# Performance work log

Hardware: AMD Instinct MI355X
Metric: run time of the kernel (lower is better)

## Reference

```python
import jax, jax.numpy as jnp
import numpy as np
import math

B, L, IN, HID, NLAYERS, AA = 16, 512, 512, 512, 6, 21
KAPPA_ADD = 5.0


def _sru_layer(x, W, v, b):
    # x: [L, B, din]; W: [din, 2*HID*k]; v, b: [2(gate f/r), 2(dir), HID]
    Lx, Bx, din = x.shape
    d = HID
    k = W.shape[1] // (2 * d)  # 4 if projecting residual, 3 if residual = input
    U = (x @ W).reshape(Lx, Bx, 2, d, k)
    res = U[..., 3] if k == 4 else x.reshape(Lx, Bx, 2, d)
    # time-flip direction 1 so a single scan handles both directions
    flip = lambda a: jnp.concatenate([a[:, :, :1], a[::-1, :, 1:]], axis=2)
    u0, u1, u2, resf = flip(U[..., 0]), flip(U[..., 1]), flip(U[..., 2]), flip(res)
    vf, vr = v[0], v[1]
    bf, br = b[0], b[1]

    def step(c, t):
        u0t, u1t, u2t, rt = t
        f = jax.nn.sigmoid(u1t + vf * c + bf)
        c1 = f * c + (1.0 - f) * u0t
        r = jax.nn.sigmoid(u2t + vr * c1 + br)
        h = r * c1 + (1.0 - r) * rt
        return c1, h

    c0 = jnp.zeros((Bx, 2, d), x.dtype)
    _, H = jax.lax.scan(step, c0, (u0, u1, u2, resf))
    return flip(H).reshape(Lx, Bx, 2 * d)


def setup_inputs():
    key = jax.random.key(0)
    inp = {}
    inp['input'] = jax.random.normal(jax.random.fold_in(key, 0), (B, L, IN), jnp.float32)
    inp['hidden'] = jnp.zeros((NLAYERS, B, 2 * HID), jnp.float32)
    for l in range(NLAYERS):
        din = IN if l == 0 else 2 * HID
        k = 4 if din != 2 * HID else 3
        inp[f'sru_w{l}'] = jax.random.normal(jax.random.fold_in(key, 10 + l), (din, 2 * HID * k), jnp.float32) * (1.0 / math.sqrt(din))
        inp[f'sru_v{l}'] = jax.random.normal(jax.random.fold_in(key, 20 + l), (2, 2, HID), jnp.float32) * 0.1
        inp[f'sru_b{l}'] = jnp.zeros((2, 2, HID), jnp.float32)

    def lin(seed, din, dout):
        w = jax.random.normal(jax.random.fold_in(key, seed), (din, dout), jnp.float32) * (1.0 / math.sqrt(din))
        return w, jnp.zeros((dout,), jnp.float32)

    inp['fc1_logits_w'], inp['fc1_logits_b'] = lin(30, 2 * HID, HID)
    inp['fc2_logits_w'], inp['fc2_logits_b'] = lin(31, HID, AA)
    inp['fc1_angles_w'], inp['fc1_angles_b'] = lin(32, 2 * HID, HID)
    inp['fc2_means_w'], inp['fc2_means_b'] = lin(33, HID, 2)
    inp['fc2_kappas_w'], inp['fc2_kappas_b'] = lin(34, HID, 2)
    return inp


def reference(input, hidden, sru_w0, sru_v0, sru_b0, sru_w1, sru_v1, sru_b1, sru_w2, sru_v2, sru_b2, sru_w3, sru_v3, sru_b3, sru_w4, sru_v4, sru_b4, sru_w5, sru_v5, sru_b5, fc1_logits_w, fc1_logits_b, fc2_logits_w, fc2_logits_b, fc1_angles_w, fc1_angles_b, fc2_means_w, fc2_means_b, fc2_kappas_w, fc2_kappas_b):
    x = input.transpose(1, 0, 2)  # [L, B, IN]
    ws = [sru_w0, sru_w1, sru_w2, sru_w3, sru_w4, sru_w5]
    vs = [sru_v0, sru_v1, sru_v2, sru_v3, sru_v4, sru_v5]
    bs = [sru_b0, sru_b1, sru_b2, sru_b3, sru_b4, sru_b5]
    for W, v, b in zip(ws, vs, bs):
        x = _sru_layer(x, W, v, b)
    sru_out = x.transpose(1, 0, 2)  # [B, L, 2*HID]
    h_log = sru_out @ fc1_logits_w + fc1_logits_b
    output_logits = jax.nn.log_softmax(h_log @ fc2_logits_w + fc2_logits_b, axis=-1)
    h_ang = sru_out @ fc1_angles_w + fc1_angles_b
    output_means = jnp.tanh(h_ang @ fc2_means_w + fc2_means_b) * math.pi
    output_kappas = KAPPA_ADD + jax.nn.softplus(h_ang @ fc2_kappas_w + fc2_kappas_b)
    return (output_logits, output_means, output_kappas)
```

## Files before the change

kernel.cpp:

```cpp
#include <hip/hip_runtime.h>

typedef __attribute__((ext_vector_type(8))) short short8;
typedef __attribute__((ext_vector_type(4))) float f32x4;

__device__ __forceinline__ ushort f2bf(float x) {
  unsigned u = __builtin_bit_cast(unsigned, x);
  u = (u + 0x7fffu + ((u >> 16) & 1u)) >> 16;
  return (ushort)u;
}
__device__ __forceinline__ float bf2f(ushort x) {
  return __builtin_bit_cast(float, ((unsigned)x) << 16);
}

#define AS1CP(p) ((const __attribute__((address_space(1))) unsigned int*)(p))
#define AS3CP(p) ((__attribute__((address_space(3))) unsigned int*)(p))
#define GLDS(g, l, SZ) __builtin_amdgcn_global_load_lds(AS1CP(g), AS3CP(l), SZ, 0, 0)

__global__ __launch_bounds__(256) void k_cvt(const float* __restrict__ in,
                                             ushort* __restrict__ out, int n4) {
  int i = blockIdx.x * 256 + threadIdx.x;
  if (i >= n4) return;
  float4 v = reinterpret_cast<const float4*>(in)[i];
  ushort4 o;
  o.x = f2bf(v.x); o.y = f2bf(v.y); o.z = f2bf(v.z); o.w = f2bf(v.w);
  reinterpret_cast<ushort4*>(out)[i] = o;
}

__global__ __launch_bounds__(256) void k_transpose(const float* __restrict__ W,
                                                   ushort* __restrict__ Wt,
                                                   int N, int K) {
  __shared__ float tile[32][33];
  int bx = blockIdx.x * 32;
  int by = blockIdx.y * 32;
  int tx = threadIdx.x, ty = threadIdx.y;
#pragma unroll
  for (int i = 0; i < 32; i += 8)
    tile[ty + i][tx] = W[(size_t)(by + ty + i) * N + bx + tx];
  __syncthreads();
#pragma unroll
  for (int i = 0; i < 32; i += 8)
    Wt[(size_t)(bx + ty + i) * K + by + tx] = f2bf(tile[tx][ty + i]);
}

template <int KKp>
__global__ __launch_bounds__(256) void k_transpose_sru(const float* __restrict__ W,
                                                       ushort* __restrict__ Wt,
                                                       int N, int K) {
  __shared__ float tile[32][33];
  int bx = blockIdx.x * 32;
  int by = blockIdx.y * 32;
  int tx = threadIdx.x, ty = threadIdx.y;
#pragma unroll
  for (int i = 0; i < 32; i += 8)
    tile[ty + i][tx] = W[(size_t)(by + ty + i) * N + bx + tx];
  __syncthreads();
#pragma unroll
  for (int i = 0; i < 32; i += 8) {
    int c = bx + ty + i;
    int ch = c / KKp, j = c - ch * KKp;
    int nc = (j < 2) ? (ch * 2 + j) : ((j == 2) ? (2048 + ch) : (3072 + ch));
    Wt[(size_t)nc * K + by + tx] = f2bf(tile[tx][ty + i]);
  }
}

template <int BF16OUT>
__global__ __launch_bounds__(256) void k_gemm(const ushort* __restrict__ A,
                                              const ushort* __restrict__ Bt,
                                              void* __restrict__ Cv,
                                              int K, int N) {
  __shared__ __align__(16) ushort lsA[2][4096];
  __shared__ __align__(16) ushort lsB[2][4096];
  const int tid = threadIdx.x;
  const int bm = blockIdx.x, bn = blockIdx.y;
  const int w = tid >> 6, l = tid & 63;
  const int wm = (w >> 1) * 64, wn = (w & 1) * 64;
  const int lr = l & 15, lg = l >> 4;
  f32x4 acc[4][4] = {};
  const int srow = tid >> 2;
  const int scol = (((tid & 3) ^ ((srow >> 1) & 3))) * 8;
  const ushort* Ag = A + (size_t)(bm * 128 + srow) * K + scol;
  const ushort* Bg = Bt + (size_t)(bn * 128 + srow) * K + scol;
  const int nt = K >> 5;
  const int rxor = (lr >> 1) & 3;

#define GEMM_ISSUE(BUF, KT)                                       \
  {                                                               \
    GLDS(Ag + (KT), &lsA[BUF][w * 512], 16);                      \
    GLDS(Ag + (size_t)64 * K + (KT), &lsA[BUF][2048 + w * 512], 16); \
    GLDS(Bg + (KT), &lsB[BUF][w * 512], 16);                      \
    GLDS(Bg + (size_t)64 * K + (KT), &lsB[BUF][2048 + w * 512], 16); \
  }

  GEMM_ISSUE(0, 0);
  for (int t = 0; t < nt; ++t) {
    const int cur = t & 1;
    if (t + 1 < nt) {
      GEMM_ISSUE(cur ^ 1, (t + 1) * 32);
      asm volatile("s_waitcnt vmcnt(4)" ::: "memory");
    } else {
      asm volatile("s_waitcnt vmcnt(0)" ::: "memory");
    }
    asm volatile("s_barrier" ::: "memory");
    short8 af[4], bfr[4];
#pragma unroll
    for (int i = 0; i < 4; ++i)
      af[i] = *(const short8*)&lsA[cur][(wm + i * 16 + lr) * 32 + ((lg ^ rxor) * 8)];
#pragma unroll
    for (int j = 0; j < 4; ++j)
      bfr[j] = *(const short8*)&lsB[cur][(wn + j * 16 + lr) * 32 + ((lg ^ rxor) * 8)];
#pragma unroll
    for (int i = 0; i < 4; ++i)
#pragma unroll
      for (int j = 0; j < 4; ++j)
        acc[i][j] = __builtin_amdgcn_mfma_f32_16x16x32_bf16(af[i], bfr[j], acc[i][j], 0, 0, 0);
    asm volatile("s_barrier" ::: "memory");
  }
#undef GEMM_ISSUE
  const size_t cbase = (size_t)(bm * 128 + wm + lg * 4) * N + bn * 128 + wn + lr;
  if (BF16OUT) {
    ushort* Cb = (ushort*)Cv + cbase;
#pragma unroll
    for (int i = 0; i < 4; ++i)
#pragma unroll
      for (int j = 0; j < 4; ++j)
#pragma unroll
        for (int r = 0; r < 4; ++r)
          Cb[(size_t)(i * 16 + r) * N + j * 16] = f2bf(acc[i][j][r]);
  } else {
    float* Cb = (float*)Cv + cbase;
#pragma unroll
    for (int i = 0; i < 4; ++i)
#pragma unroll
      for (int j = 0; j < 4; ++j)
#pragma unroll
        for (int r = 0; r < 4; ++r)
          Cb[(size_t)(i * 16 + r) * N + j * 16] = acc[i][j][r];
  }
}

__global__ __launch_bounds__(64, 1) void sru_rec6(const ushort* __restrict__ U, int NU,
                                                  const ushort* __restrict__ R, int RS,
                                                  const float* __restrict__ v,
                                                  const float* __restrict__ bb,
                                                  ushort* __restrict__ H) {
  const int lane = threadIdx.x;
  if (lane >= 16) return;
  const int blk = blockIdx.x;
  const int b = blk >> 6, rem = blk & 63, dir = rem >> 5;
  const int ch = dir * 512 + ((rem & 31) << 4) + lane;
  const float vf = v[ch], vr = v[1024 + ch];
  const float bfv = bb[ch], brv = bb[1024 + ch];
  const float vfn = -vf, vrn = -vr;
  const float kf0 = -bfv, kr0 = -brv;
  const int tstep = dir ? -1 : 1;
  const int t0 = dir ? 511 : 0;
  const ushort* U01 = U + (size_t)b * 512 * NU + ch * 2;
  const ushort* U2  = U + (size_t)b * 512 * NU + 2048 + ch;
  const ushort* Rb  = R + (size_t)b * 512 * RS + ch;
  ushort* Hb = H + (size_t)b * 512 * 1024 + ch;

  unsigned q01[4][8];
  ushort q2[4][8], qr[4][8];

#define SR_ISSUE(J, TI)                                                        \
  {                                                                            \
    const int base_ = (TI) * 8;                                                \
    _Pragma("unroll")                                                          \
    for (int t = 0; t < 8; ++t) {                                              \
      int tt = t0 + tstep * (base_ + t);                                       \
      q01[J][t] = *(const unsigned*)(U01 + (size_t)tt * NU);                   \
      q2[J][t] = U2[(size_t)tt * NU];                                          \
      qr[J][t] = Rb[(size_t)tt * RS];                                          \
    }                                                                          \
  }

#define SR_COMP(J, TI)                                                         \
  {                                                                            \
    _Pragma("unroll")                                                          \
    for (int s = 0; s < 8; ++s) {                                              \
      float u0 = bf2f((ushort)(q01[J][s] & 0xffffu));                          \
      float u1 = bf2f((ushort)(q01[J][s] >> 16));                              \
      float u2 = bf2f(q2[J][s]);                                               \
      float uR = bf2f(qr[J][s]);                                               \
      float ef = __expf(__builtin_fmaf(vfn, c, kf0 - u1));                     \
      float f = __builtin_amdgcn_rcpf(1.f + ef);                               \
      c = __builtin_fmaf(f, c - u0, u0);                                       \
      float er = __expf(__builtin_fmaf(vrn, c, kr0 - u2));                     \
      float r = __builtin_amdgcn_rcpf(1.f + er);                               \
      float hh = __builtin_fmaf(r, c - uR, uR);                                \
      Hb[(size_t)(t0 + tstep * ((TI) * 8 + s)) * 1024] = f2bf(hh);             \
    }                                                                          \
  }

#define SR_W32 asm volatile("s_waitcnt vmcnt(32)" ::: "memory");

  SR_ISSUE(0, 0)
  SR_ISSUE(1, 1)
  float c = 0.f;
  asm volatile("s_waitcnt vmcnt(24)" ::: "memory");
  SR_ISSUE(2, 2) SR_COMP(0, 0)
  SR_W32 SR_ISSUE(3, 3) SR_COMP(1, 1)
  SR_W32 SR_ISSUE(0, 4) SR_COMP(2, 2)
  SR_W32 SR_ISSUE(1, 5) SR_COMP(3, 3)
#pragma unroll 1
  for (int ii = 1; ii <= 14; ++ii) {
#define TILE_J(J)                                                              \
    {                                                                          \
      const int i = ii * 4 + (J);                                              \
      SR_W32                                                                   \
      SR_ISSUE((((J) + 2) & 3), i + 2)                                         \
      SR_COMP(J, i)                                                            \
    }
    TILE_J(0) TILE_J(1) TILE_J(2) TILE_J(3)
#undef TILE_J
  }
  SR_W32 SR_ISSUE(2, 62) SR_COMP(0, 60)
  SR_W32 SR_ISSUE(3, 63) SR_COMP(1, 61)
  SR_W32 SR_COMP(2, 62)
  asm volatile("s_waitcnt vmcnt(8)" ::: "memory");
  SR_COMP(3, 63)
#undef SR_ISSUE
#undef SR_COMP
#undef SR_W32
}

__global__ __launch_bounds__(256) void k_buildW2(const float* __restrict__ w2l,
                                                 const float* __restrict__ w2m,
                                                 const float* __restrict__ w2k,
                                                 ushort* __restrict__ Wt2) {
  int i = blockIdx.x * 256 + threadIdx.x;
  if (i >= 128 * 1024) return;
  int n = i >> 10, k = i & 1023;
  float vv = 0.f;
  if (n < 21 && k < 512) vv = w2l[k * 21 + n];
  else if (n >= 21 && n < 23 && k >= 512) vv = w2m[(k - 512) * 2 + (n - 21)];
  else if (n >= 23 && n < 25 && k >= 512) vv = w2k[(k - 512) * 2 + (n - 23)];
  Wt2[i] = f2bf(vv);
}

__global__ __launch_bounds__(64) void k_bias25(const float* __restrict__ b1l,
                                               const float* __restrict__ b1a,
                                               const float* __restrict__ w2l,
                                               const float* __restrict__ b2l,
                                               const float* __restrict__ w2m,
                                               const float* __restrict__ b2m,
                                               const float* __restrict__ w2k,
                                               const float* __restrict__ b2k,
                                               float* __restrict__ b2adj) {
  int o = threadIdx.x;
  if (o >= 25) return;
  float s;
  if (o < 21) {
    s = b2l[o];
    for (int k = 0; k < 512; ++k) s += b1l[k] * w2l[k * 21 + o];
  } else if (o < 23) {
    s = b2m[o - 21];
    for (int k = 0; k < 512; ++k) s += b1a[k] * w2m[k * 2 + (o - 21)];
  } else {
    s = b2k[o - 23];
    for (int k = 0; k < 512; ++k) s += b1a[k] * w2k[k * 2 + (o - 23)];
  }
  b2adj[o] = s;
}

__global__ __launch_bounds__(64) void k_act(const float* __restrict__ T,
                                            const float* __restrict__ b2adj,
                                            float* __restrict__ out) {
  const int row = blockIdx.x;
  const int lane = threadIdx.x;
  float myv = 0.f;
  if (lane < 25) myv = T[(size_t)row * 128 + lane] + b2adj[lane];
  float x = (lane < 21) ? myv : -1e30f;
#pragma unroll
  for (int off = 32; off; off >>= 1) x = fmaxf(x, __shfl_xor(x, off));
  float e = (lane < 21) ? expf(myv - x) : 0.f;
#pragma unroll
  for (int off = 32; off; off >>= 1) e += __shfl_xor(e, off);
  float lse = x + logf(e);
  if (lane < 21) {
    out[(size_t)row * 21 + lane] = myv - lse;
  } else if (lane < 23) {
    out[172032 + row * 2 + (lane - 21)] = tanhf(myv) * 3.14159265358979323846f;
  } else if (lane < 25) {
    float sp = (myv > 20.f) ? myv : log1pf(expf(myv));
    out[188416 + row * 2 + (lane - 23)] = 5.f + sp;
  }
}

extern "C" void kernel_launch(void* const* d_in, const int* in_sizes, int n_in,
                              void* d_out, int out_size, void* d_ws, size_t ws_size,
                              hipStream_t stream) {
  (void)in_sizes; (void)n_in; (void)out_size; (void)ws_size;
  const float* input = (const float*)d_in[0];
  const float* sw[6]; const float* sv[6]; const float* sb[6];
  for (int l = 0; l < 6; ++l) {
    sw[l] = (const float*)d_in[2 + 3 * l];
    sv[l] = (const float*)d_in[3 + 3 * l];
    sb[l] = (const float*)d_in[4 + 3 * l];
  }
  const float* fc1lw = (const float*)d_in[20];
  const float* fc1lb = (const float*)d_in[21];
  const float* fc2lw = (const float*)d_in[22];
  const float* fc2lb = (const float*)d_in[23];
  const float* fc1aw = (const float*)d_in[24];
  const float* fc1ab = (const float*)d_in[25];
  const float* fc2mw = (const float*)d_in[26];
  const float* fc2mb = (const float*)d_in[27];
  const float* fc2kw = (const float*)d_in[28];
  const float* fc2kb = (const float*)d_in[29];

  char* ws = (char*)d_ws;
  ushort* U = (ushort*)ws;
  ushort* Hcat2 = (ushort*)ws;
  float* T = (float*)(ws + 67108864);
  ushort* H0 = (ushort*)(ws + 134217728);
  ushort* H1 = (ushort*)(ws + 150994944);
  ushort* X0 = (ushort*)(ws + 167772160);
  const size_t wbase = 176160768;
  ushort* Wtl[6];
  Wtl[0] = (ushort*)(ws + wbase);
  for (int l = 1; l < 6; ++l)
    Wtl[l] = (ushort*)(ws + wbase + 4194304 + (size_t)(l - 1) * 6291456);
  ushort* Wfc = (ushort*)(ws + wbase + 4194304 + 5ull * 6291456);
  ushort* Wt2 = (ushort*)(ws + wbase + 37748736);
  float* b2adj = (float*)(ws + wbase + 38010880);

  k_cvt<<<4096, 256, 0, stream>>>(input, X0, 8192 * 512 / 4);
  k_buildW2<<<512, 256, 0, stream>>>(fc2lw, fc2mw, fc2kw, Wt2);
  k_bias25<<<1, 64, 0, stream>>>(fc1lb, fc1ab, fc2lw, fc2lb, fc2mw, fc2mb,
                                 fc2kw, fc2kb, b2adj);

  k_transpose_sru<4><<<dim3(128, 16), dim3(32, 8), 0, stream>>>(sw[0], Wtl[0], 4096, 512);
  for (int l = 1; l < 6; ++l)
    k_transpose_sru<3><<<dim3(96, 32), dim3(32, 8), 0, stream>>>(sw[l], Wtl[l], 3072, 1024);
  k_transpose<<<dim3(16, 32), dim3(32, 8), 0, stream>>>(fc1lw, Wfc, 512, 1024);
  k_transpose<<<dim3(16, 32), dim3(32, 8), 0, stream>>>(fc1aw, Wfc + (size_t)512 * 1024, 512, 1024);

  for (int l = 0; l < 6; ++l) {
    const ushort* Ain = (l == 0) ? X0 : ((l & 1) ? H0 : H1);
    ushort* Hout = (l & 1) ? H1 : H0;
    int K = (l == 0) ? 512 : 1024;
    int N = (l == 0) ? 4096 : 3072;
    k_gemm<1><<<dim3(64, N / 128), 256, 0, stream>>>(Ain, Wtl[l], U, K, N);
    if (l == 0)
      sru_rec6<<<1024, 64, 0, stream>>>(U, 4096, U + 3072, 4096, sv[l], sb[l], Hout);
    else
      sru_rec6<<<1024, 64, 0, stream>>>(U, 3072, Ain, 1024, sv[l], sb[l], Hout);
  }

  k_gemm<1><<<dim3(64, 8), 256, 0, stream>>>(H1, Wfc, Hcat2, 1024, 1024);

  k_gemm<0><<<dim3(64, 1), 256, 0, stream>>>(Hcat2, Wt2, T, 1024, 128);

  k_act<<<8192, 64, 0, stream>>>(T, b2adj, (float*)d_out);
}
```

Before: 886.1 us.

## Use all 64 lanes per wave in SRU recurrence and deepen load prefetch

The recurrence kernel now assigns 64 channels per wavefront instead of 16 (1024 blocks with 48 idle lanes become 256 fully used blocks). The software prefetch distance rises from two to three 8-step tiles, with a vmcnt(63) wait and a reworked epilogue drain. The bf16 unpack of u0/u1 uses shift and mask instead of the ushort conversion. The aim is wider coalesced loads and stores per wave and more latency hiding. The cost is fewer waves in flight across the GPU (256 vs 1024) and tighter reliance on the hand-written waitcnt counts.

```diff
diff --git a/kernel.cpp b/kernel.cpp
--- a/kernel.cpp
+++ b/kernel.cpp
@@ -138,16 +138,15 @@
   }
 }
 
-__global__ __launch_bounds__(64, 1) void sru_rec6(const ushort* __restrict__ U, int NU,
+__global__ __launch_bounds__(64, 1) void sru_rec8(const ushort* __restrict__ U, int NU,
                                                   const ushort* __restrict__ R, int RS,
                                                   const float* __restrict__ v,
                                                   const float* __restrict__ bb,
                                                   ushort* __restrict__ H) {
   const int lane = threadIdx.x;
-  if (lane >= 16) return;
   const int blk = blockIdx.x;
-  const int b = blk >> 6, rem = blk & 63, dir = rem >> 5;
-  const int ch = dir * 512 + ((rem & 31) << 4) + lane;
+  const int b = blk >> 4, rem = blk & 15, dir = rem >> 3, cg = rem & 7;
+  const int ch = dir * 512 + cg * 64 + lane;
   const float vf = v[ch], vr = v[1024 + ch];
   const float bfv = bb[ch], brv = bb[1024 + ch];
   const float vfn = -vf, vrn = -vr;
@@ -178,8 +177,8 @@
   {                                                                            \
     _Pragma("unroll")                                                          \
     for (int s = 0; s < 8; ++s) {                                              \
-      float u0 = bf2f((ushort)(q01[J][s] & 0xffffu));                          \
-      float u1 = bf2f((ushort)(q01[J][s] >> 16));                              \
+      float u0 = __builtin_bit_cast(float, q01[J][s] << 16);                   \
+      float u1 = __builtin_bit_cast(float, q01[J][s] & 0xffff0000u);           \
       float u2 = bf2f(q2[J][s]);                                               \
       float uR = bf2f(qr[J][s]);                                               \
       float ef = __expf(__builtin_fmaf(vfn, c, kf0 - u1));                     \
@@ -192,36 +191,33 @@
     }                                                                          \
   }
 
-#define SR_W32 asm volatile("s_waitcnt vmcnt(32)" ::: "memory");
-
   SR_ISSUE(0, 0)
   SR_ISSUE(1, 1)
+  SR_ISSUE(2, 2)
   float c = 0.f;
-  asm volatile("s_waitcnt vmcnt(24)" ::: "memory");
-  SR_ISSUE(2, 2) SR_COMP(0, 0)
-  SR_W32 SR_ISSUE(3, 3) SR_COMP(1, 1)
-  SR_W32 SR_ISSUE(0, 4) SR_COMP(2, 2)
-  SR_W32 SR_ISSUE(1, 5) SR_COMP(3, 3)
 #pragma unroll 1
-  for (int ii = 1; ii <= 14; ++ii) {
+  for (int ii = 0; ii < 15; ++ii) {
 #define TILE_J(J)                                                              \
     {                                                                          \
       const int i = ii * 4 + (J);                                              \
-      SR_W32                                                                   \
-      SR_ISSUE((((J) + 2) & 3), i + 2)                                         \
+      SR_ISSUE((((J) + 3) & 3), i + 3)                                         \
+      asm volatile("s_waitcnt vmcnt(63)" ::: "memory");                        \
       SR_COMP(J, i)                                                            \
     }
     TILE_J(0) TILE_J(1) TILE_J(2) TILE_J(3)
 #undef TILE_J
   }
-  SR_W32 SR_ISSUE(2, 62) SR_COMP(0, 60)
-  SR_W32 SR_ISSUE(3, 63) SR_COMP(1, 61)
-  SR_W32 SR_COMP(2, 62)
-  asm volatile("s_waitcnt vmcnt(8)" ::: "memory");
+  SR_ISSUE(3, 63)
+  asm volatile("s_waitcnt vmcnt(63)" ::: "memory");
+  SR_COMP(0, 60)
+  asm volatile("s_waitcnt vmcnt(48)" ::: "memory");
+  SR_COMP(1, 61)
+  asm volatile("s_waitcnt vmcnt(24)" ::: "memory");
+  SR_COMP(2, 62)
+  asm volatile("s_waitcnt vmcnt(0)" ::: "memory");
   SR_COMP(3, 63)
 #undef SR_ISSUE
 #undef SR_COMP
-#undef SR_W32
 }
 
 __global__ __launch_bounds__(256) void k_buildW2(const float* __restrict__ w2l,
@@ -343,9 +339,9 @@
     int N = (l == 0) ? 4096 : 3072;
     k_gemm<1><<<dim3(64, N / 128), 256, 0, stream>>>(Ain, Wtl[l], U, K, N);
     if (l == 0)
-      sru_rec6<<<1024, 64, 0, stream>>>(U, 4096, U + 3072, 4096, sv[l], sb[l], Hout);
+      sru_rec8<<<256, 64, 0, stream>>>(U, 4096, U + 3072, 4096, sv[l], sb[l], Hout);
     else
-      sru_rec6<<<1024, 64, 0, stream>>>(U, 3072, Ain, 1024, sv[l], sb[l], Hout);
+      sru_rec8<<<256, 64, 0, stream>>>(U, 3072, Ain, 1024, sv[l], sb[l], Hout);
   }
 
   k_gemm<1><<<dim3(64, 8), 256, 0, stream>>>(H1, Wfc, Hcat2, 1024, 1024);
```

New measurement: 769.6 us. 13.2% less time.
